# Kernel tuning notes

Hardware: AMD Instinct MI355X
Metric: run time of the kernel (lower is better)

## Reference

```python
import jax, jax.numpy as jnp
import numpy as np

B, S, E = 2, 2048, 2048
H, KV, D = 16, 4, 128
G = H // KV
ROPE_THETA = 10000.0


def setup_inputs() -> dict:
    key = jax.random.key(0)
    ks = jax.random.split(key, 8)
    std = 0.02
    return {
        "x": jax.random.normal(ks[0], (B, S, E), jnp.float32),
        "Wq": jax.random.normal(ks[1], (H * D, E), jnp.float32) * std,
        "bq": jax.random.normal(ks[2], (H * D,), jnp.float32) * std,
        "Wk": jax.random.normal(ks[3], (KV * D, E), jnp.float32) * std,
        "bk": jax.random.normal(ks[4], (KV * D,), jnp.float32) * std,
        "Wv": jax.random.normal(ks[5], (KV * D, E), jnp.float32) * std,
        "bv": jax.random.normal(ks[6], (KV * D,), jnp.float32) * std,
        "Wo": jax.random.normal(ks[7], (E, H * D), jnp.float32) * std,
    }


def _rope_cos_sin(seq_len, head_dim):
    inv_freq = 1.0 / (ROPE_THETA ** (jnp.arange(0, head_dim, 2, dtype=jnp.float32) / head_dim))
    pos = jnp.arange(seq_len, dtype=jnp.float32)  # rope scale factor = 1.0
    freqs = pos[:, None] * inv_freq[None, :]        # [S, D/2]
    emb = jnp.concatenate([freqs, freqs], axis=-1)  # [S, D]
    return jnp.cos(emb), jnp.sin(emb)


def _apply_rope(t, cos, sin):
    # t: [..., S, <extra dims>, D]; cos/sin: [S, D] broadcast over extra dims
    half = t.shape[-1] // 2
    extra = t.ndim - 3  # dims between S (axis 1) and D (last)
    c = cos.reshape((1, cos.shape[0]) + (1,) * extra + (cos.shape[1],))
    s = sin.reshape((1, sin.shape[0]) + (1,) * extra + (sin.shape[1],))
    rot = jnp.concatenate([-t[..., half:], t[..., :half]], axis=-1)
    return t * c + rot * s


def reference(x, Wq, bq, Wk, bk, Wv, bv, Wo):
    b, s, e = x.shape
    # QKV projections (biases on q/k/v, none on o)
    q = (jnp.einsum("bse,he->bsh", x, Wq) + bq).reshape(b, s, KV, G, D)
    k = (jnp.einsum("bse,he->bsh", x, Wk) + bk).reshape(b, s, KV, D)
    v = (jnp.einsum("bse,he->bsh", x, Wv) + bv).reshape(b, s, KV, D)

    cos, sin = _rope_cos_sin(s, D)
    q = _apply_rope(q, cos, sin)
    k = _apply_rope(k, cos, sin)

    scale = 1.0 / jnp.sqrt(jnp.float32(D))
    # GQA: q heads grouped per kv head; k/v broadcast over group dim
    scores = jnp.einsum("bskgd,btkd->bkgst", q, k) * scale  # [B,KV,G,S,S]
    causal = jnp.tril(jnp.ones((s, s), dtype=bool))
    scores = jnp.where(causal, scores, jnp.float32(-1e9))
    attn = jax.nn.softmax(scores, axis=-1)
    out = jnp.einsum("bkgst,btkd->bskgd", attn, v).reshape(b, s, H * D)
    return jnp.einsum("bsh,eh->bse", out, Wo)
```

## Files before the change

kernel.cpp:

```cpp
#include <hip/hip_runtime.h>
#include <hip/hip_bf16.h>
#include <math.h>

#define BB 2
#define SS 2048
#define EE 2048
#define HH 16
#define KVH 4
#define DD 128
#define QTILES 32

typedef short short8 __attribute__((ext_vector_type(8)));
typedef float f32x4 __attribute__((ext_vector_type(4)));

__device__ __forceinline__ unsigned int f2bf1(float x) {
    union { float f; unsigned int u; } v; v.f = x;
    return (v.u + 0x7FFFu + ((v.u >> 16) & 1u)) >> 16;
}
__device__ __forceinline__ unsigned int packbf(float a, float b) {
    return f2bf1(a) | (f2bf1(b) << 16);
}
__device__ __forceinline__ void gl_lds16(const void* g, void* l) {
    __builtin_amdgcn_global_load_lds(
        (const __attribute__((address_space(1))) unsigned int*)g,
        (__attribute__((address_space(3))) unsigned int*)l,
        16, 0, 0);
}

__global__ __launch_bounds__(256) void cvt_all_kernel(
    const float* __restrict__ x,  const float* __restrict__ Wq,
    const float* __restrict__ Wk, const float* __restrict__ Wv,
    const float* __restrict__ Wo, const float* __restrict__ bq,
    const float* __restrict__ bk, const float* __restrict__ bv,
    unsigned short* __restrict__ xb, unsigned short* __restrict__ wqkv,
    unsigned short* __restrict__ wob, float* __restrict__ bqkv,
    float* __restrict__ rtab)
{
    long id = (long)blockIdx.x * 256 + threadIdx.x;
    const float* src; unsigned short* dst; long j;
    if (id < 2097152)      { j = id;           src = x;  dst = xb; }
    else if (id < 3145728) { j = id - 2097152; src = Wq; dst = wqkv; }
    else if (id < 3407872) { j = id - 3145728; src = Wk; dst = wqkv + 4194304; }
    else if (id < 3670016) { j = id - 3407872; src = Wv; dst = wqkv + 5242880; }
    else if (id < 4718592) { j = id - 3670016; src = Wo; dst = wob; }
    else if (id < 4719360) {
        long c = (id - 4718592) * 4;
#pragma unroll
        for (int e = 0; e < 4; ++e) {
            long cc = c + e;
            bqkv[cc] = (cc < 2048) ? bq[cc] : (cc < 2560 ? bk[cc - 2048] : bv[cc - 2560]);
        }
        return;
    } else if (id < 4850432) {
        long e = id - 4719360;
        int sg = (int)(e >> 6);
        int dg = (int)(e & 63);
        float inv_freq = expf(-(float)dg * (logf(10000.0f) / 64.0f));
        float fr = (float)sg * inv_freq;
        rtab[e]          = cosf(fr);
        rtab[131072 + e] = sinf(fr);
        return;
    } else return;
    float4 f = ((const float4*)src)[j];
    ((uint2*)dst)[j] = make_uint2(packbf(f.x, f.y), packbf(f.z, f.w));
}

template <bool OUT_BF16>
__global__ __launch_bounds__(256) void gemm_mfma_kernel(
    const unsigned short* __restrict__ A, const unsigned short* __restrict__ W,
    const float* __restrict__ bias, void* __restrict__ Cout,
    int M, int N, int K)
{
    __shared__ unsigned short As[128 * 64];
    __shared__ unsigned short Bs[128 * 64];

    const int tid  = threadIdx.x;
    const int w    = tid >> 6;
    const int lane = tid & 63;
    const int quad = lane >> 4;
    const int l16  = lane & 15;
    const int wr   = w >> 1, wc = w & 1;
    const int m0 = blockIdx.y * 128, n0 = blockIdx.x * 128;

    f32x4 acc[4][4];
#pragma unroll
    for (int i = 0; i < 4; ++i)
#pragma unroll
        for (int j = 0; j < 4; ++j) acc[i][j] = (f32x4){0.f, 0.f, 0.f, 0.f};

    const int scol = ((lane & 7) ^ (lane >> 3)) * 8;
    const unsigned short* Ag = A + (size_t)(m0 + w * 8 + (lane >> 3)) * K + scol;
    const unsigned short* Wg = W + (size_t)(n0 + w * 8 + (lane >> 3)) * K + scol;
    unsigned short* AsB = &As[(w * 8) * 64];
    unsigned short* BsB = &Bs[(w * 8) * 64];

    const int rkey = (l16 & 7) * 8;

    for (int k0 = 0; k0 < K; k0 += 64) {
#pragma unroll
        for (int c = 0; c < 4; ++c) {
            gl_lds16(Ag + k0 + (size_t)(32 * c) * K, AsB + 32 * c * 64);
            gl_lds16(Wg + k0 + (size_t)(32 * c) * K, BsB + 32 * c * 64);
        }
        __syncthreads();

#pragma unroll
        for (int ks = 0; ks < 2; ++ks) {
            short8 a_f[4], b_f[4];
#pragma unroll
            for (int i = 0; i < 4; ++i)
                a_f[i] = *(const short8*)&As[(wr * 64 + i * 16 + l16) * 64 + (((ks * 4 + quad) * 8) ^ rkey)];
#pragma unroll
            for (int j = 0; j < 4; ++j)
                b_f[j] = *(const short8*)&Bs[(wc * 64 + j * 16 + l16) * 64 + (((ks * 4 + quad) * 8) ^ rkey)];
#pragma unroll
            for (int i = 0; i < 4; ++i)
#pragma unroll
                for (int j = 0; j < 4; ++j)
                    acc[i][j] = __builtin_amdgcn_mfma_f32_16x16x32_bf16(a_f[i], b_f[j], acc[i][j], 0, 0, 0);
        }
        __syncthreads();
    }

    float bj[4];
#pragma unroll
    for (int j = 0; j < 4; ++j)
        bj[j] = bias ? bias[n0 + wc * 64 + j * 16 + l16] : 0.0f;
#pragma unroll
    for (int i = 0; i < 4; ++i) {
#pragma unroll
        for (int r = 0; r < 4; ++r) {
            size_t row = m0 + wr * 64 + i * 16 + quad * 4 + r;
#pragma unroll
            for (int j = 0; j < 4; ++j) {
                size_t col = n0 + wc * 64 + j * 16 + l16;
                float val = acc[i][j][r] + bj[j];
                if (OUT_BF16)
                    ((unsigned short*)Cout)[row * N + col] = (unsigned short)f2bf1(val);
                else
                    ((float*)Cout)[row * N + col] = val;
            }
        }
    }
}

__global__ __launch_bounds__(256) void rope_k_kernel(
    unsigned short* __restrict__ qkv,
    const float* __restrict__ ctab, const float* __restrict__ stab)
{
    const int m = blockIdx.x;
    const int s = m & (SS - 1);
    const int hh = threadIdx.x >> 6;
    const int d  = threadIdx.x & 63;
    unsigned short* p = qkv + (size_t)m * 3072 + 2048 + hh * 128;
    float c  = ctab[s * 64 + d];
    float sn = stab[s * 64 + d];
    union { unsigned int u; float f; } x1, x2;
    x1.u = ((unsigned int)p[d]) << 16;
    x2.u = ((unsigned int)p[d + 64]) << 16;
    p[d]      = (unsigned short)f2bf1(x1.f * c - x2.f * sn);
    p[d + 64] = (unsigned short)f2bf1(x2.f * c + x1.f * sn);
}

__global__ __launch_bounds__(256, 2) void attn_mfma_kernel(
    const unsigned short* __restrict__ qkv, unsigned short* __restrict__ o,
    const float* __restrict__ ctab, const float* __restrict__ stab)
{
    __shared__ unsigned int Ks_u[2][64 * 64];
    __shared__ unsigned int Vs_u[2][128 * 32];
    __shared__ unsigned short Ps[4][16 * 64];

    const int tid  = threadIdx.x;
    const int w    = tid >> 6;
    const int lane = tid & 63;
    const int quad = lane >> 4;
    const int l16  = lane & 15;
    const int jpair = blockIdx.x;
    const int h     = blockIdx.y;
    const int b     = blockIdx.z;
    const int kv    = h >> 2;

    const float k2 = 0.12752789744920764f;

    const unsigned short* kbase = qkv + (size_t)b * SS * 3072 + 2048 + kv * 128;
    const unsigned short* vbase = kbase + 512;

    const int kc  = tid & 15;
    const int kp0 = tid >> 4;
    const int vpp = tid >> 3;
    const int vd0 = (tid & 7) * 16;

    for (int pass = 0; pass < 2; ++pass) {
        const int qt = pass ? (QTILES - 1 - jpair) : jpair;
        const int q0 = qt * 64;

        short8 qf[4];
        {
            const unsigned short* qp = qkv + (size_t)(b * SS + q0 + w * 16 + l16) * 3072 + h * 128 + quad * 8;
#pragma unroll
            for (int ks = 0; ks < 4; ++ks)
                qf[ks] = *(const short8*)(qp + ks * 32);
            const int s = q0 + w * 16 + l16;
            const float* cr = ctab + s * 64;
            const float* sr = stab + s * 64;
#pragma unroll
            for (int ks = 0; ks < 2; ++ks) {
#pragma unroll
                for (int j = 0; j < 8; ++j) {
                    int d = quad * 8 + ks * 32 + j;
                    float c  = cr[d];
                    float sn = sr[d];
                    union { unsigned int u; float f; } lo, hi;
                    lo.u = ((unsigned int)(unsigned short)qf[ks][j]) << 16;
                    hi.u = ((unsigned int)(unsigned short)qf[ks + 2][j]) << 16;
                    qf[ks][j]     = (short)(unsigned short)f2bf1(lo.f * c - hi.f * sn);
                    qf[ks + 2][j] = (short)(unsigned short)f2bf1(hi.f * c + lo.f * sn);
                }
            }
        }

        uint4 kpre[4], vpa[2], vpb[2];
        {
            const unsigned short* kg = kbase + (size_t)kp0 * 3072 + kc * 8;
#pragma unroll
            for (int rr = 0; rr < 4; ++rr)
                kpre[rr] = *(const uint4*)(kg + (size_t)rr * 16 * 3072);
            const unsigned short* vg = vbase + (size_t)(2 * vpp) * 3072 + vd0;
            vpa[0] = *(const uint4*)(vg);
            vpa[1] = *(const uint4*)(vg + 8);
            vpb[0] = *(const uint4*)(vg + 3072);
            vpb[1] = *(const uint4*)(vg + 3072 + 8);
        }

        float m_r[4], l_r[4];
        f32x4 Oacc[8];
#pragma unroll
        for (int r = 0; r < 4; ++r) { m_r[r] = -1e30f; l_r[r] = 0.0f; }
#pragma unroll
        for (int ot = 0; ot < 8; ++ot) Oacc[ot] = (f32x4){0.f, 0.f, 0.f, 0.f};

        for (int t = 0; t <= qt; ++t) {
            const int buf = t & 1;
            unsigned int* Kb = Ks_u[buf];
            unsigned int* Vb = Vs_u[buf];

#pragma unroll
            for (int rr = 0; rr < 4; ++rr) {
                int pos = kp0 + rr * 16;
                int key = (kp0 + rr) & 7;
                *(uint4*)&Kb[pos * 64 + (kc ^ key) * 4] = kpre[rr];
            }
            {
                const unsigned int* pa = (const unsigned int*)vpa;
                const unsigned int* pb = (const unsigned int*)vpb;
#pragma unroll
                for (int j = 0; j < 8; ++j) {
                    unsigned lo = __builtin_amdgcn_perm(pb[j], pa[j], 0x05040100);
                    unsigned hi = __builtin_amdgcn_perm(pb[j], pa[j], 0x07060302);
                    int d0 = vd0 + 2 * j;
                    int g  = d0 >> 4;
                    int k0 = (d0 + g) & 7;
                    int k1 = (d0 + 1 + g) & 7;
                    Vb[d0 * 32 + (((vpp >> 2) ^ k0) & 7) * 4 + (vpp & 3)] = lo;
                    Vb[(d0 + 1) * 32 + (((vpp >> 2) ^ k1) & 7) * 4 + (vpp & 3)] = hi;
                }
            }

            if (t < qt) {
                const unsigned short* kg = kbase + (size_t)((t + 1) * 64 + kp0) * 3072 + kc * 8;
#pragma unroll
                for (int rr = 0; rr < 4; ++rr)
                    kpre[rr] = *(const uint4*)(kg + (size_t)rr * 16 * 3072);
                const unsigned short* vg = vbase + (size_t)((t + 1) * 64 + 2 * vpp) * 3072 + vd0;
                vpa[0] = *(const uint4*)(vg);
                vpa[1] = *(const uint4*)(vg + 8);
                vpb[0] = *(const uint4*)(vg + 3072);
                vpb[1] = *(const uint4*)(vg + 3072 + 8);
            }
            __syncthreads();

            f32x4 S[4];
#pragma unroll
            for (int ct = 0; ct < 4; ++ct) {
                f32x4 s = (f32x4){0.f, 0.f, 0.f, 0.f};
                const int row = ct * 16 + l16;
                const int key = (l16 + ct) & 7;
#pragma unroll
                for (int ks = 0; ks < 4; ++ks) {
                    short8 kf = *(const short8*)&Kb[row * 64 + ((ks * 4 + quad) ^ key) * 4];
                    s = __builtin_amdgcn_mfma_f32_16x16x32_bf16(qf[ks], kf, s, 0, 0, 0);
                }
                S[ct] = s;
            }

            if (t == qt) {
                const int rowloc = w * 16 + quad * 4;
#pragma unroll
                for (int ct = 0; ct < 4; ++ct)
#pragma unroll
                    for (int r = 0; r < 4; ++r)
                        if (ct * 16 + l16 > rowloc + r) S[ct][r] = -1e30f;
            }

            float c0[4];
#pragma unroll
            for (int r = 0; r < 4; ++r)
                c0[r] = fmaxf(fmaxf(S[0][r], S[1][r]), fmaxf(S[2][r], S[3][r]));
#pragma unroll
            for (int st = 1; st <= 8; st <<= 1)
#pragma unroll
                for (int r = 0; r < 4; ++r)
                    c0[r] = fmaxf(c0[r], __shfl_xor(c0[r], st));
            float alpha[4], mh[4], rs[4];
#pragma unroll
            for (int r = 0; r < 4; ++r) {
                float mnew = fmaxf(m_r[r], c0[r]);
                alpha[r] = exp2f((m_r[r] - mnew) * k2);
                m_r[r] = mnew;
                mh[r] = mnew * k2;
                rs[r] = 0.0f;
            }
#pragma unroll
            for (int r = 0; r < 4; ++r) {
                const int prow = quad * 4 + r;
                const int pkey = (prow >> 2) ^ ((prow & 3) << 1);
#pragma unroll
                for (int ct = 0; ct < 4; ++ct) {
                    float p = exp2f(S[ct][r] * k2 - mh[r]);
                    rs[r] += p;
                    int chunk = ct * 2 + (l16 >> 3);
                    union { float f; unsigned u; } pu; pu.f = p;
                    Ps[w][prow * 64 + (chunk ^ pkey) * 8 + (l16 & 7)] =
                        (unsigned short)((pu.u + 0x8000u) >> 16);
                }
            }
#pragma unroll
            for (int st = 1; st <= 8; st <<= 1)
#pragma unroll
                for (int r = 0; r < 4; ++r)
                    rs[r] += __shfl_xor(rs[r], st);
#pragma unroll
            for (int r = 0; r < 4; ++r) {
                l_r[r] = l_r[r] * alpha[r] + rs[r];
#pragma unroll
                for (int ot = 0; ot < 8; ++ot) Oacc[ot][r] *= alpha[r];
            }

            {
                const int pkeyr = (l16 >> 2) ^ ((l16 & 3) << 1);
                short8 pf0 = *(const short8*)&Ps[w][l16 * 64 + (quad ^ pkeyr) * 8];
                short8 pf1 = *(const short8*)&Ps[w][l16 * 64 + ((4 + quad) ^ pkeyr) * 8];
#pragma unroll
                for (int ot = 0; ot < 8; ++ot) {
                    const int d = ot * 16 + l16;
                    const int vkey = (l16 + ot) & 7;
                    short8 v0 = *(const short8*)&Vb[d * 32 + (quad ^ vkey) * 4];
                    Oacc[ot] = __builtin_amdgcn_mfma_f32_16x16x32_bf16(pf0, v0, Oacc[ot], 0, 0, 0);
                    short8 v1 = *(const short8*)&Vb[d * 32 + ((4 + quad) ^ vkey) * 4];
                    Oacc[ot] = __builtin_amdgcn_mfma_f32_16x16x32_bf16(pf1, v1, Oacc[ot], 0, 0, 0);
                }
            }
        }

        float inv[4];
#pragma unroll
        for (int r = 0; r < 4; ++r) inv[r] = 1.0f / l_r[r];
        const int orow0 = q0 + w * 16 + quad * 4;
        unsigned short* ob = o + (size_t)(b * SS + orow0) * 2048 + h * 128 + l16;
#pragma unroll
        for (int r = 0; r < 4; ++r)
#pragma unroll
            for (int ot = 0; ot < 8; ++ot)
                ob[(size_t)r * 2048 + ot * 16] = (unsigned short)f2bf1(Oacc[ot][r] * inv[r]);

        __syncthreads();
    }
}

extern "C" void kernel_launch(void* const* d_in, const int* in_sizes, int n_in,
                              void* d_out, int out_size, void* d_ws, size_t ws_size,
                              hipStream_t stream)
{
    const float* x  = (const float*)d_in[0];
    const float* Wq = (const float*)d_in[1];
    const float* bq = (const float*)d_in[2];
    const float* Wk = (const float*)d_in[3];
    const float* bk = (const float*)d_in[4];
    const float* Wv = (const float*)d_in[5];
    const float* bv = (const float*)d_in[6];
    const float* Wo = (const float*)d_in[7];
    float* out = (float*)d_out;

    const int M = BB * SS;
    char* wsb = (char*)d_ws;
    unsigned short* xb   = (unsigned short*)wsb;  wsb += (size_t)M * EE * 2;
    unsigned short* wqkv = (unsigned short*)wsb;  wsb += (size_t)3072 * EE * 2;
    unsigned short* wob  = (unsigned short*)wsb;  wsb += (size_t)EE * EE * 2;
    unsigned short* qkvb = (unsigned short*)wsb;  wsb += (size_t)M * 3072 * 2;
    unsigned short* abb  = (unsigned short*)wsb;  wsb += (size_t)M * 2048 * 2;
    float* bqkv = (float*)wsb;                    wsb += 4096 * 4;
    float* rtab = (float*)wsb;

    cvt_all_kernel<<<18947, 256, 0, stream>>>(x, Wq, Wk, Wv, Wo, bq, bk, bv,
                                              xb, wqkv, wob, bqkv, rtab);

    gemm_mfma_kernel<true><<<dim3(3072 / 128, M / 128), 256, 0, stream>>>(
        xb, wqkv, bqkv, qkvb, M, 3072, EE);

    rope_k_kernel<<<M, 256, 0, stream>>>(qkvb, rtab, rtab + 131072);

    attn_mfma_kernel<<<dim3(16, HH, BB), 256, 0, stream>>>(
        qkvb, abb, rtab, rtab + 131072);

    gemm_mfma_kernel<false><<<dim3(EE / 128, M / 128), 256, 0, stream>>>(
        abb, wob, nullptr, out, M, EE, 2048);
}
```

Baseline: 349.6 us.

## Process paired long/short query tiles in one KV sweep to share K/V loads

```diff
diff --git a/kernel.cpp b/kernel.cpp
--- a/kernel.cpp
+++ b/kernel.cpp
@@ -175,10 +175,12 @@
     const int lane = tid & 63;
     const int quad = lane >> 4;
     const int l16  = lane & 15;
-    const int jpair = blockIdx.x;
-    const int h     = blockIdx.y;
-    const int b     = blockIdx.z;
-    const int kv    = h >> 2;
+    const int h    = blockIdx.y;
+    const int b    = blockIdx.z;
+    const int jp   = (b == 0) ? blockIdx.x : (15 - blockIdx.x);
+    const int kv   = h >> 2;
+    const int qtL  = QTILES - 1 - jp;
+    const int qtS  = jp;
 
     const float k2 = 0.12752789744920764f;
 
@@ -190,94 +192,100 @@
     const int vpp = tid >> 3;
     const int vd0 = (tid & 7) * 16;
 
-    for (int pass = 0; pass < 2; ++pass) {
-        const int qt = pass ? (QTILES - 1 - jpair) : jpair;
-        const int q0 = qt * 64;
-
-        short8 qf[4];
+    short8 qf[2][4];
+#pragma unroll
+    for (int qi = 0; qi < 2; ++qi) {
+        const int q0 = (qi == 0 ? qtL : qtS) * 64;
+        const unsigned short* qp = qkv + (size_t)(b * SS + q0 + w * 16 + l16) * 3072 + h * 128 + quad * 8;
+#pragma unroll
+        for (int ks = 0; ks < 4; ++ks)
+            qf[qi][ks] = *(const short8*)(qp + ks * 32);
+        const int s = q0 + w * 16 + l16;
+        const float* cr = ctab + s * 64;
+        const float* sr = stab + s * 64;
+#pragma unroll
+        for (int ks = 0; ks < 2; ++ks) {
+#pragma unroll
+            for (int j = 0; j < 8; ++j) {
+                int d = quad * 8 + ks * 32 + j;
+                float c  = cr[d];
+                float sn = sr[d];
+                union { unsigned int u; float f; } lo, hi;
+                lo.u = ((unsigned int)(unsigned short)qf[qi][ks][j]) << 16;
+                hi.u = ((unsigned int)(unsigned short)qf[qi][ks + 2][j]) << 16;
+                qf[qi][ks][j]     = (short)(unsigned short)f2bf1(lo.f * c - hi.f * sn);
+                qf[qi][ks + 2][j] = (short)(unsigned short)f2bf1(hi.f * c + lo.f * sn);
+            }
+        }
+    }
+
+    uint4 kpre[4], vpa[2], vpb[2];
+    {
+        const unsigned short* kg = kbase + (size_t)kp0 * 3072 + kc * 8;
+#pragma unroll
+        for (int rr = 0; rr < 4; ++rr)
+            kpre[rr] = *(const uint4*)(kg + (size_t)rr * 16 * 3072);
+        const unsigned short* vg = vbase + (size_t)(2 * vpp) * 3072 + vd0;
+        vpa[0] = *(const uint4*)(vg);
+        vpa[1] = *(const uint4*)(vg + 8);
+        vpb[0] = *(const uint4*)(vg + 3072);
+        vpb[1] = *(const uint4*)(vg + 3072 + 8);
+    }
+
+    float m_r[2][4], l_r[2][4];
+    f32x4 Oacc[2][8];
+#pragma unroll
+    for (int qi = 0; qi < 2; ++qi) {
+#pragma unroll
+        for (int r = 0; r < 4; ++r) { m_r[qi][r] = -1e30f; l_r[qi][r] = 0.0f; }
+#pragma unroll
+        for (int ot = 0; ot < 8; ++ot) Oacc[qi][ot] = (f32x4){0.f, 0.f, 0.f, 0.f};
+    }
+
+    for (int t = 0; t <= qtL; ++t) {
+        const int buf = t & 1;
+        unsigned int* Kb = Ks_u[buf];
+        unsigned int* Vb = Vs_u[buf];
+
+#pragma unroll
+        for (int rr = 0; rr < 4; ++rr) {
+            int pos = kp0 + rr * 16;
+            int key = (kp0 + rr) & 7;
+            *(uint4*)&Kb[pos * 64 + (kc ^ key) * 4] = kpre[rr];
+        }
         {
-            const unsigned short* qp = qkv + (size_t)(b * SS + q0 + w * 16 + l16) * 3072 + h * 128 + quad * 8;
-#pragma unroll
-            for (int ks = 0; ks < 4; ++ks)
-                qf[ks] = *(const short8*)(qp + ks * 32);
-            const int s = q0 + w * 16 + l16;
-            const float* cr = ctab + s * 64;
-            const float* sr = stab + s * 64;
-#pragma unroll
-            for (int ks = 0; ks < 2; ++ks) {
-#pragma unroll
-                for (int j = 0; j < 8; ++j) {
-                    int d = quad * 8 + ks * 32 + j;
-                    float c  = cr[d];
-                    float sn = sr[d];
-                    union { unsigned int u; float f; } lo, hi;
-                    lo.u = ((unsigned int)(unsigned short)qf[ks][j]) << 16;
-                    hi.u = ((unsigned int)(unsigned short)qf[ks + 2][j]) << 16;
-                    qf[ks][j]     = (short)(unsigned short)f2bf1(lo.f * c - hi.f * sn);
-                    qf[ks + 2][j] = (short)(unsigned short)f2bf1(hi.f * c + lo.f * sn);
-                }
-            }
-        }
-
-        uint4 kpre[4], vpa[2], vpb[2];
-        {
-            const unsigned short* kg = kbase + (size_t)kp0 * 3072 + kc * 8;
+            const unsigned int* pa = (const unsigned int*)vpa;
+            const unsigned int* pb = (const unsigned int*)vpb;
+#pragma unroll
+            for (int j = 0; j < 8; ++j) {
+                unsigned lo = __builtin_amdgcn_perm(pb[j], pa[j], 0x05040100);
+                unsigned hi = __builtin_amdgcn_perm(pb[j], pa[j], 0x07060302);
+                int d0 = vd0 + 2 * j;
+                int g  = d0 >> 4;
+                int k0 = (d0 + g) & 7;
+                int k1 = (d0 + 1 + g) & 7;
+                Vb[d0 * 32 + (((vpp >> 2) ^ k0) & 7) * 4 + (vpp & 3)] = lo;
+                Vb[(d0 + 1) * 32 + (((vpp >> 2) ^ k1) & 7) * 4 + (vpp & 3)] = hi;
+            }
+        }
+
+        if (t < qtL) {
+            const unsigned short* kg = kbase + (size_t)((t + 1) * 64 + kp0) * 3072 + kc * 8;
 #pragma unroll
             for (int rr = 0; rr < 4; ++rr)
                 kpre[rr] = *(const uint4*)(kg + (size_t)rr * 16 * 3072);
-            const unsigned short* vg = vbase + (size_t)(2 * vpp) * 3072 + vd0;
+            const unsigned short* vg = vbase + (size_t)((t + 1) * 64 + 2 * vpp) * 3072 + vd0;
             vpa[0] = *(const uint4*)(vg);
             vpa[1] = *(const uint4*)(vg + 8);
             vpb[0] = *(const uint4*)(vg + 3072);
             vpb[1] = *(const uint4*)(vg + 3072 + 8);
         }
-
-        float m_r[4], l_r[4];
-        f32x4 Oacc[8];
-#pragma unroll
-        for (int r = 0; r < 4; ++r) { m_r[r] = -1e30f; l_r[r] = 0.0f; }
-#pragma unroll
-        for (int ot = 0; ot < 8; ++ot) Oacc[ot] = (f32x4){0.f, 0.f, 0.f, 0.f};
-
-        for (int t = 0; t <= qt; ++t) {
-            const int buf = t & 1;
-            unsigned int* Kb = Ks_u[buf];
-            unsigned int* Vb = Vs_u[buf];
-
-#pragma unroll
-            for (int rr = 0; rr < 4; ++rr) {
-                int pos = kp0 + rr * 16;
-                int key = (kp0 + rr) & 7;
-                *(uint4*)&Kb[pos * 64 + (kc ^ key) * 4] = kpre[rr];
-            }
-            {
-                const unsigned int* pa = (const unsigned int*)vpa;
-                const unsigned int* pb = (const unsigned int*)vpb;
-#pragma unroll
-                for (int j = 0; j < 8; ++j) {
-                    unsigned lo = __builtin_amdgcn_perm(pb[j], pa[j], 0x05040100);
-                    unsigned hi = __builtin_amdgcn_perm(pb[j], pa[j], 0x07060302);
-                    int d0 = vd0 + 2 * j;
-                    int g  = d0 >> 4;
-                    int k0 = (d0 + g) & 7;
-                    int k1 = (d0 + 1 + g) & 7;
-                    Vb[d0 * 32 + (((vpp >> 2) ^ k0) & 7) * 4 + (vpp & 3)] = lo;
-                    Vb[(d0 + 1) * 32 + (((vpp >> 2) ^ k1) & 7) * 4 + (vpp & 3)] = hi;
-                }
-            }
-
-            if (t < qt) {
-                const unsigned short* kg = kbase + (size_t)((t + 1) * 64 + kp0) * 3072 + kc * 8;
-#pragma unroll
-                for (int rr = 0; rr < 4; ++rr)
-                    kpre[rr] = *(const uint4*)(kg + (size_t)rr * 16 * 3072);
-                const unsigned short* vg = vbase + (size_t)((t + 1) * 64 + 2 * vpp) * 3072 + vd0;
-                vpa[0] = *(const uint4*)(vg);
-                vpa[1] = *(const uint4*)(vg + 8);
-                vpb[0] = *(const uint4*)(vg + 3072);
-                vpb[1] = *(const uint4*)(vg + 3072 + 8);
-            }
-            __syncthreads();
+        __syncthreads();
+
+#pragma unroll
+        for (int qi = 0; qi < 2; ++qi) {
+            if (qi == 1 && t > qtS) break;
+            const int tqt = (qi == 0) ? qtL : qtS;
 
             f32x4 S[4];
 #pragma unroll
@@ -288,12 +296,12 @@
 #pragma unroll
                 for (int ks = 0; ks < 4; ++ks) {
                     short8 kf = *(const short8*)&Kb[row * 64 + ((ks * 4 + quad) ^ key) * 4];
-                    s = __builtin_amdgcn_mfma_f32_16x16x32_bf16(qf[ks], kf, s, 0, 0, 0);
+                    s = __builtin_amdgcn_mfma_f32_16x16x32_bf16(qf[qi][ks], kf, s, 0, 0, 0);
                 }
                 S[ct] = s;
             }
 
-            if (t == qt) {
+            if (t == tqt) {
                 const int rowloc = w * 16 + quad * 4;
 #pragma unroll
                 for (int ct = 0; ct < 4; ++ct)
@@ -314,9 +322,9 @@
             float alpha[4], mh[4], rs[4];
 #pragma unroll
             for (int r = 0; r < 4; ++r) {
-                float mnew = fmaxf(m_r[r], c0[r]);
-                alpha[r] = exp2f((m_r[r] - mnew) * k2);
-                m_r[r] = mnew;
+                float mnew = fmaxf(m_r[qi][r], c0[r]);
+                alpha[r] = exp2f((m_r[qi][r] - mnew) * k2);
+                m_r[qi][r] = mnew;
                 mh[r] = mnew * k2;
                 rs[r] = 0.0f;
             }
@@ -341,9 +349,9 @@
                     rs[r] += __shfl_xor(rs[r], st);
 #pragma unroll
             for (int r = 0; r < 4; ++r) {
-                l_r[r] = l_r[r] * alpha[r] + rs[r];
-#pragma unroll
-                for (int ot = 0; ot < 8; ++ot) Oacc[ot][r] *= alpha[r];
+                l_r[qi][r] = l_r[qi][r] * alpha[r] + rs[r];
+#pragma unroll
+                for (int ot = 0; ot < 8; ++ot) Oacc[qi][ot][r] *= alpha[r];
             }
 
             {
@@ -355,25 +363,27 @@
                     const int d = ot * 16 + l16;
                     const int vkey = (l16 + ot) & 7;
                     short8 v0 = *(const short8*)&Vb[d * 32 + (quad ^ vkey) * 4];
-                    Oacc[ot] = __builtin_amdgcn_mfma_f32_16x16x32_bf16(pf0, v0, Oacc[ot], 0, 0, 0);
+                    Oacc[qi][ot] = __builtin_amdgcn_mfma_f32_16x16x32_bf16(pf0, v0, Oacc[qi][ot], 0, 0, 0);
                     short8 v1 = *(const short8*)&Vb[d * 32 + ((4 + quad) ^ vkey) * 4];
-                    Oacc[ot] = __builtin_amdgcn_mfma_f32_16x16x32_bf16(pf1, v1, Oacc[ot], 0, 0, 0);
+                    Oacc[qi][ot] = __builtin_amdgcn_mfma_f32_16x16x32_bf16(pf1, v1, Oacc[qi][ot], 0, 0, 0);
                 }
             }
         }
-
+    }
+
+#pragma unroll
+    for (int qi = 0; qi < 2; ++qi) {
+        const int q0 = (qi == 0 ? qtL : qtS) * 64;
         float inv[4];
 #pragma unroll
-        for (int r = 0; r < 4; ++r) inv[r] = 1.0f / l_r[r];
+        for (int r = 0; r < 4; ++r) inv[r] = 1.0f / l_r[qi][r];
         const int orow0 = q0 + w * 16 + quad * 4;
         unsigned short* ob = o + (size_t)(b * SS + orow0) * 2048 + h * 128 + l16;
 #pragma unroll
         for (int r = 0; r < 4; ++r)
 #pragma unroll
             for (int ot = 0; ot < 8; ++ot)
-                ob[(size_t)r * 2048 + ot * 16] = (unsigned short)f2bf1(Oacc[ot][r] * inv[r]);
-
-        __syncthreads();
+                ob[(size_t)r * 2048 + ot * 16] = (unsigned short)f2bf1(Oacc[qi][ot][r] * inv[r]);
     }
 }
 
```

Measured after the change: 355.4 us. Within noise of the previous version (+1.7%).
